# Performance work log

Measured on AMD Instinct MI355X. Metric: run time of the kernel, lower is better.

Reference implementation:

```python
import jax, jax.numpy as jnp
import numpy as np
import math

B, S, D, H = 2, 2048, 1024, 16
DK = D // H

def setup_inputs() -> dict:
    key = jax.random.key(0)
    ks = jax.random.split(key, 12)
    sc = 1.0 / math.sqrt(D)
    q = jax.random.normal(ks[0], (B, S, D), jnp.float32)
    k = jax.random.normal(ks[1], (B, S, D), jnp.float32)
    v = jax.random.normal(ks[2], (B, S, D), jnp.float32)
    # causal mask, broadcast over batch and heads; 0 -> masked (filled with -100)
    mask = jnp.tril(jnp.ones((S, S), jnp.int32))[None, None, :, :]
    w_q = jax.random.normal(ks[3], (D, D), jnp.float32) * sc
    b_q = jnp.zeros((D,), jnp.float32)
    w_k = jax.random.normal(ks[4], (D, D), jnp.float32) * sc
    b_k = jnp.zeros((D,), jnp.float32)
    w_v = jax.random.normal(ks[5], (D, D), jnp.float32) * sc
    b_v = jnp.zeros((D,), jnp.float32)
    w_0 = jax.random.normal(ks[6], (D, D), jnp.float32) * sc
    b_0 = jnp.zeros((D,), jnp.float32)
    return {"q": q, "k": k, "v": v, "mask": mask,
            "w_q": w_q, "b_q": b_q, "w_k": w_k, "b_k": b_k,
            "w_v": w_v, "b_v": b_v, "w_0": w_0, "b_0": b_0}

def reference(q, k, v, mask, w_q, b_q, w_k, b_k, w_v, b_v, w_0, b_0):
    # projections (nn.Linear: x @ W^T + b)
    query = q @ w_q.T + b_q              # [B,S,D]
    key_ = k @ w_k.T + b_k
    value = v @ w_v.T + b_v
    # split heads -> [B,H,S,DK]
    def split(x):
        return x.reshape(B, S, H, DK).transpose(0, 2, 1, 3)
    Q, K, V = split(query), split(key_), split(value)
    scores = jnp.einsum('bhqd,bhkd->bhqk', Q, K) / math.sqrt(DK)
    scores = jnp.where(mask == 0, jnp.float32(-100.0), scores)
    attn = jax.nn.softmax(scores, axis=-1)   # dropout p=0.0 -> identity
    out = jnp.einsum('bhqk,bhkd->bhqd', attn, V)  # [B,H,S,DK]
    out = out.transpose(0, 2, 1, 3).reshape(B, S, D)
    return out @ w_0.T + b_0
```

## Files before the change

### kernel.cpp

```cpp
#include <hip/hip_runtime.h>


namespace {

typedef unsigned short u16;
typedef short bf16x8 __attribute__((ext_vector_type(8)));
typedef float f32x4 __attribute__((ext_vector_type(4)));

constexpr int Bz = 2, Sq = 2048, Dm = 1024, Hh = 16, Dk = 64;
constexpr int Mr = Bz * Sq;

__device__ __forceinline__ u16 bf_rne(float f, float* hif) {
  unsigned u = __float_as_uint(f);
  unsigned r = (u + 0x7fffu + ((u >> 16) & 1u)) >> 16;
  if (hif) *hif = __uint_as_float(r << 16);
  return (u16)r;
}

__device__ __forceinline__ void global_load_lds16(const u16* g, u16* lds) {
  __builtin_amdgcn_global_load_lds(
      (const __attribute__((address_space(1))) void*)g,
      (__attribute__((address_space(3))) void*)lds, 16, 0, 0);
}

struct ConvArgs {
  const float* s[7]; u16* hi[7]; u16* lo[7]; int n[7];
};

__global__ __launch_bounds__(256)
void convert_hilo(ConvArgs a) {
  const int z = blockIdx.y;
  const int n = a.n[z];
  const int i = (blockIdx.x * 256 + threadIdx.x) * 4;
  if (i >= n) return;
  const float4 v = *(const float4*)(a.s[z] + i);
  float hf;
  ushort4 h, l;
  h.x = bf_rne(v.x, &hf); l.x = bf_rne(v.x - hf, nullptr);
  h.y = bf_rne(v.y, &hf); l.y = bf_rne(v.y - hf, nullptr);
  h.z = bf_rne(v.z, &hf); l.z = bf_rne(v.z - hf, nullptr);
  h.w = bf_rne(v.w, &hf); l.w = bf_rne(v.w - hf, nullptr);
  *(ushort4*)(a.hi[z] + i) = h;
  *(ushort4*)(a.lo[z] + i) = l;
}

template<int OUT>
__device__ __forceinline__ void gemm_split_body(
    const u16* __restrict__ Ahi, const u16* __restrict__ Alo,
    const u16* __restrict__ Bhi, const u16* __restrict__ Blo,
    const float* __restrict__ bias, float scale,
    u16* __restrict__ Yh, u16* __restrict__ Yl, float* __restrict__ Yf)
{
  constexpr int K = 1024;
  __shared__ u16 lAh[4096], lAl[4096], lBh[4096], lBl[4096];

  const int t = threadIdx.x;
  const int w = t >> 6, l = t & 63;
  const int m0 = blockIdx.x * 128, n0 = blockIdx.y * 128;
  const int wm = (w >> 1) * 64, wn = (w & 1) * 64;
  const int kg = l >> 4, lr = l & 15;

  f32x4 acc[4][4] = {};

  for (int k0 = 0; k0 < K; k0 += 32) {
#pragma unroll
    for (int is = 0; is < 2; ++is) {
      const int s = is * 256 + w * 64 + l;
      const int row = s & 127, g = s >> 7;
      const size_t aoff = (size_t)(m0 + row) * K + k0 + g * 8;
      const size_t boff = (size_t)(n0 + row) * K + k0 + g * 8;
      const int ldso = (is * 256 + w * 64) * 8;
      global_load_lds16(Ahi + aoff, &lAh[ldso]);
      global_load_lds16(Alo + aoff, &lAl[ldso]);
      global_load_lds16(Bhi + boff, &lBh[ldso]);
      global_load_lds16(Blo + boff, &lBl[ldso]);
    }
    __syncthreads();

    bf16x8 ah[4], al[4], bh[4], bl[4];
#pragma unroll
    for (int f = 0; f < 4; ++f) {
      const int ai = kg * 1024 + (wm + f * 16 + lr) * 8;
      const int bi = kg * 1024 + (wn + f * 16 + lr) * 8;
      ah[f] = *(const bf16x8*)&lAh[ai];
      al[f] = *(const bf16x8*)&lAl[ai];
      bh[f] = *(const bf16x8*)&lBh[bi];
      bl[f] = *(const bf16x8*)&lBl[bi];
    }
#pragma unroll
    for (int mf = 0; mf < 4; ++mf)
#pragma unroll
      for (int nf = 0; nf < 4; ++nf) {
        acc[mf][nf] = __builtin_amdgcn_mfma_f32_16x16x32_bf16(ah[mf], bh[nf], acc[mf][nf], 0, 0, 0);
        acc[mf][nf] = __builtin_amdgcn_mfma_f32_16x16x32_bf16(ah[mf], bl[nf], acc[mf][nf], 0, 0, 0);
        acc[mf][nf] = __builtin_amdgcn_mfma_f32_16x16x32_bf16(al[mf], bh[nf], acc[mf][nf], 0, 0, 0);
      }
    __syncthreads();
  }

#pragma unroll
  for (int mf = 0; mf < 4; ++mf)
#pragma unroll
    for (int nf = 0; nf < 4; ++nf) {
      const int n = n0 + wn + nf * 16 + lr;
      const float bv = bias[n];
#pragma unroll
      for (int r = 0; r < 4; ++r) {
        const int mm = m0 + wm + mf * 16 + kg * 4 + r;
        const float val = (acc[mf][nf][r] + bv) * scale;
        if (OUT == 2) {
          Yf[(size_t)mm * Dm + n] = val;
        } else {
          float hf;
          const u16 hi = bf_rne(val, &hf);
          const u16 lo = bf_rne(val - hf, nullptr);
          const int bb = mm >> 11, ss = mm & (Sq - 1);
          const int hh = n >> 6, dkk = n & (Dk - 1);
          size_t idx;
          if (OUT == 0) idx = ((size_t)(bb * Hh + hh) * Sq + ss) * Dk + dkk;
          else          idx = ((size_t)(bb * Hh + hh) * Dk + dkk) * Sq + ss;
          Yh[idx] = hi; Yl[idx] = lo;
        }
      }
    }
}

__global__ __launch_bounds__(256, 2)
void gemm_qkv_split(const u16* xqh, const u16* xql, const u16* xkh, const u16* xkl,
                    const u16* xvh, const u16* xvl,
                    const u16* wqh, const u16* wql, const u16* wkh, const u16* wkl,
                    const u16* wvh, const u16* wvl,
                    const float* bq, const float* bk, const float* bv,
                    u16* Qhi, u16* Qlo, u16* Khi, u16* Klo, u16* Vthi, u16* Vtlo)
{
  const int z = blockIdx.z;
  if (z == 0)
    gemm_split_body<0>(xqh, xql, wqh, wql, bq, 0.125f, Qhi, Qlo, nullptr);
  else if (z == 1)
    gemm_split_body<0>(xkh, xkl, wkh, wkl, bk, 1.0f, Khi, Klo, nullptr);
  else
    gemm_split_body<1>(xvh, xvl, wvh, wvl, bv, 1.0f, Vthi, Vtlo, nullptr);
}

__global__ __launch_bounds__(256, 2)
void gemm_out_split(const u16* Ah, const u16* Al, const u16* Bh, const u16* Bl,
                    const float* bias, float* Y)
{
  gemm_split_body<2>(Ah, Al, Bh, Bl, bias, 1.0f, nullptr, nullptr, Y);
}

__global__ __launch_bounds__(256, 2)
void attn_mfma(const u16* __restrict__ Qhi, const u16* __restrict__ Qlo,
               const u16* __restrict__ Khi, const u16* __restrict__ Klo,
               const u16* __restrict__ Vthi, const u16* __restrict__ Vtlo,
               u16* __restrict__ ctxh, u16* __restrict__ ctxl)
{
  __shared__ u16 stg[2 * 8192];
  __shared__ float Pld[4][16][36];

  const int qt = blockIdx.x, h = blockIdx.y, b = blockIdx.z;
  const int w = threadIdx.x >> 6, l = threadIdx.x & 63;
  const int lr = l & 15, g = l >> 4;
  const int q0 = qt * 64;
  const size_t hoff  = (size_t)(b * Hh + h) * Sq * Dk;
  const size_t hofft = (size_t)(b * Hh + h) * Dk * Sq;

  bf16x8 qh[2], ql[2];
  {
    const size_t qrow = hoff + (size_t)(q0 + 4 * lr + w) * Dk;
    qh[0] = *(const bf16x8*)(Qhi + qrow + 8 * g);
    qh[1] = *(const bf16x8*)(Qhi + qrow + 32 + 8 * g);
    ql[0] = *(const bf16x8*)(Qlo + qrow + 8 * g);
    ql[1] = *(const bf16x8*)(Qlo + qrow + 32 + 8 * g);
  }

  const int NT = 2 * (qt + 1);

  auto stage = [&](int t, int bb) {
    const int k0 = t * 32;
    u16* dst = stg + bb * 8192 + (w * 256) * 8;
#pragma unroll
    for (int jj = 0; jj < 4; ++jj) {
      const int s = jj * 64 + l;
      const u16* gp;
      if (w == 0)      gp = Khi  + hoff  + (size_t)(k0 + (s & 31)) * Dk + (s >> 5) * 8;
      else if (w == 1) gp = Klo  + hoff  + (size_t)(k0 + (s & 31)) * Dk + (s >> 5) * 8;
      else if (w == 2) gp = Vthi + hofft + (size_t)(s & 63) * Sq + k0 + (s >> 6) * 8;
      else             gp = Vtlo + hofft + (size_t)(s & 63) * Sq + k0 + (s >> 6) * 8;
      global_load_lds16(gp, dst + jj * 64 * 8);
    }
  };

  f32x4 O[4] = {};
  float m[4]    = {-1e30f, -1e30f, -1e30f, -1e30f};
  float lsum[4] = {0.f, 0.f, 0.f, 0.f};

  stage(0, 0);
  __syncthreads();

  for (int t = 0; t < NT; ++t) {
    const int bb = t & 1;
    const int k0 = t * 32;
    if (t + 1 < NT) stage(t + 1, bb ^ 1);

    const u16* sb = stg + bb * 8192;

    bf16x8 kh[2][2], kl[2][2];
#pragma unroll
    for (int c = 0; c < 2; ++c)
#pragma unroll
      for (int h16 = 0; h16 < 2; ++h16) {
        const int slot = (c * 4 + g) * 32 + h16 * 16 + lr;
        kh[h16][c] = *(const bf16x8*)(sb + slot * 8);
        kl[h16][c] = *(const bf16x8*)(sb + (256 + slot) * 8);
      }

    f32x4 Sv[2] = {};
#pragma unroll
    for (int c = 0; c < 2; ++c) {
      Sv[0] = __builtin_amdgcn_mfma_f32_16x16x32_bf16(qh[c], kh[0][c], Sv[0], 0, 0, 0);
      Sv[0] = __builtin_amdgcn_mfma_f32_16x16x32_bf16(qh[c], kl[0][c], Sv[0], 0, 0, 0);
      Sv[0] = __builtin_amdgcn_mfma_f32_16x16x32_bf16(ql[c], kh[0][c], Sv[0], 0, 0, 0);
      Sv[1] = __builtin_amdgcn_mfma_f32_16x16x32_bf16(qh[c], kh[1][c], Sv[1], 0, 0, 0);
      Sv[1] = __builtin_amdgcn_mfma_f32_16x16x32_bf16(qh[c], kl[1][c], Sv[1], 0, 0, 0);
      Sv[1] = __builtin_amdgcn_mfma_f32_16x16x32_bf16(ql[c], kh[1][c], Sv[1], 0, 0, 0);
    }

    if (k0 + 31 >= q0) {
#pragma unroll
      for (int h16 = 0; h16 < 2; ++h16) {
        const int kv = k0 + h16 * 16 + lr;
#pragma unroll
        for (int reg = 0; reg < 4; ++reg) {
          const int qq = q0 + 4 * (4 * g + reg) + w;
          if (kv > qq) Sv[h16][reg] = -3.0e38f;
        }
      }
    }

    float tmax[4], corr[4];
#pragma unroll
    for (int reg = 0; reg < 4; ++reg) tmax[reg] = fmaxf(Sv[0][reg], Sv[1][reg]);
#pragma unroll
    for (int d = 1; d < 16; d <<= 1)
#pragma unroll
      for (int reg = 0; reg < 4; ++reg)
        tmax[reg] = fmaxf(tmax[reg], __shfl_xor(tmax[reg], d));
#pragma unroll
    for (int reg = 0; reg < 4; ++reg) {
      const float mn = fmaxf(m[reg], tmax[reg]);
      corr[reg] = __expf(m[reg] - mn);
      m[reg] = mn;
    }
    f32x4 P0, P1;
    float psum[4];
#pragma unroll
    for (int reg = 0; reg < 4; ++reg) {
      P0[reg] = __expf(Sv[0][reg] - m[reg]);
      P1[reg] = __expf(Sv[1][reg] - m[reg]);
      psum[reg] = P0[reg] + P1[reg];
    }
#pragma unroll
    for (int d = 1; d < 16; d <<= 1)
#pragma unroll
      for (int reg = 0; reg < 4; ++reg)
        psum[reg] += __shfl_xor(psum[reg], d);
#pragma unroll
    for (int reg = 0; reg < 4; ++reg)
      lsum[reg] = lsum[reg] * corr[reg] + psum[reg];
#pragma unroll
    for (int dt = 0; dt < 4; ++dt)
#pragma unroll
      for (int reg = 0; reg < 4; ++reg)
        O[dt][reg] *= corr[reg];

#pragma unroll
    for (int reg = 0; reg < 4; ++reg) {
      Pld[w][4 * g + reg][lr]      = P0[reg];
      Pld[w][4 * g + reg][16 + lr] = P1[reg];
    }
    asm volatile("s_waitcnt lgkmcnt(0)" ::: "memory");
    float pa[8];
    *(float4*)&pa[0] = *(const float4*)&Pld[w][lr][8 * g];
    *(float4*)&pa[4] = *(const float4*)&Pld[w][lr][8 * g + 4];

    bf16x8 pah, pal;
#pragma unroll
    for (int j = 0; j < 8; ++j) {
      float hf;
      pah[j] = (short)bf_rne(pa[j], &hf);
      pal[j] = (short)bf_rne(pa[j] - hf, nullptr);
    }

#pragma unroll
    for (int dt = 0; dt < 4; ++dt) {
      const int vslot = 512 + g * 64 + dt * 16 + lr;
      const bf16x8 vh = *(const bf16x8*)(sb + vslot * 8);
      const bf16x8 vl = *(const bf16x8*)(sb + (vslot + 256) * 8);
      O[dt] = __builtin_amdgcn_mfma_f32_16x16x32_bf16(pah, vh, O[dt], 0, 0, 0);
      O[dt] = __builtin_amdgcn_mfma_f32_16x16x32_bf16(pah, vl, O[dt], 0, 0, 0);
      O[dt] = __builtin_amdgcn_mfma_f32_16x16x32_bf16(pal, vh, O[dt], 0, 0, 0);
    }

    __syncthreads();
  }

  float inv[4];
#pragma unroll
  for (int reg = 0; reg < 4; ++reg) inv[reg] = 1.0f / lsum[reg];
#pragma unroll
  for (int dt = 0; dt < 4; ++dt)
#pragma unroll
    for (int reg = 0; reg < 4; ++reg) {
      const int qq = q0 + 4 * (4 * g + reg) + w;
      const float o = O[dt][reg] * inv[reg];
      float hf;
      const u16 hi = bf_rne(o, &hf);
      const u16 lo = bf_rne(o - hf, nullptr);
      const size_t idx = ((size_t)(b * Sq + qq) << 10) + h * Dk + dt * 16 + lr;
      ctxh[idx] = hi;
      ctxl[idx] = lo;
    }
}

}

extern "C" void kernel_launch(void* const* d_in, const int* in_sizes, int n_in,
                              void* d_out, int out_size, void* d_ws, size_t ws_size,
                              hipStream_t stream)
{
  (void)in_sizes; (void)n_in; (void)out_size;

  const float* q   = (const float*)d_in[0];
  const float* k   = (const float*)d_in[1];
  const float* v   = (const float*)d_in[2];
  const float* w_q = (const float*)d_in[4];
  const float* b_q = (const float*)d_in[5];
  const float* w_k = (const float*)d_in[6];
  const float* b_k = (const float*)d_in[7];
  const float* w_v = (const float*)d_in[8];
  const float* b_v = (const float*)d_in[9];
  const float* w_0 = (const float*)d_in[10];
  const float* b_0 = (const float*)d_in[11];
  float* out = (float*)d_out;

  const size_t MB = 1024 * 1024;
  const size_t NACT = (size_t)Mr * Dm;
  const size_t NW   = (size_t)Dm * Dm;
  if (ws_size < 112 * MB) return;

  char* ws = (char*)d_ws;
  u16* xqh = (u16*)(ws + 0*MB);  u16* xql = (u16*)(ws + 8*MB);
  u16* xkh = (u16*)(ws + 16*MB); u16* xkl = (u16*)(ws + 24*MB);
  u16* xvh = (u16*)(ws + 32*MB); u16* xvl = (u16*)(ws + 40*MB);
  u16* ctxh = (u16*)(ws + 0*MB); u16* ctxl = (u16*)(ws + 8*MB);
  u16* wqh = (u16*)(ws + 48*MB); u16* wql = (u16*)(ws + 50*MB);
  u16* wkh = (u16*)(ws + 52*MB); u16* wkl = (u16*)(ws + 54*MB);
  u16* wvh = (u16*)(ws + 56*MB); u16* wvl = (u16*)(ws + 58*MB);
  u16* w0h = (u16*)(ws + 60*MB); u16* w0l = (u16*)(ws + 62*MB);
  u16* Qhi  = (u16*)(ws + 64*MB); u16* Qlo  = (u16*)(ws + 72*MB);
  u16* Khi  = (u16*)(ws + 80*MB); u16* Klo  = (u16*)(ws + 88*MB);
  u16* Vthi = (u16*)(ws + 96*MB); u16* Vtlo = (u16*)(ws + 104*MB);

  ConvArgs ca;
  ca.s[0] = q;   ca.hi[0] = xqh; ca.lo[0] = xql; ca.n[0] = (int)NACT;
  ca.s[1] = k;   ca.hi[1] = xkh; ca.lo[1] = xkl; ca.n[1] = (int)NACT;
  ca.s[2] = v;   ca.hi[2] = xvh; ca.lo[2] = xvl; ca.n[2] = (int)NACT;
  ca.s[3] = w_q; ca.hi[3] = wqh; ca.lo[3] = wql; ca.n[3] = (int)NW;
  ca.s[4] = w_k; ca.hi[4] = wkh; ca.lo[4] = wkl; ca.n[4] = (int)NW;
  ca.s[5] = w_v; ca.hi[5] = wvh; ca.lo[5] = wvl; ca.n[5] = (int)NW;
  ca.s[6] = w_0; ca.hi[6] = w0h; ca.lo[6] = w0l; ca.n[6] = (int)NW;

  convert_hilo<<<dim3(NACT / 1024, 7), 256, 0, stream>>>(ca);

  gemm_qkv_split<<<dim3(Mr / 128, Dm / 128, 3), 256, 0, stream>>>(
      xqh, xql, xkh, xkl, xvh, xvl,
      wqh, wql, wkh, wkl, wvh, wvl,
      b_q, b_k, b_v, Qhi, Qlo, Khi, Klo, Vthi, Vtlo);

  attn_mfma<<<dim3(Sq / 64, Hh, Bz), 256, 0, stream>>>(
      Qhi, Qlo, Khi, Klo, Vthi, Vtlo, ctxh, ctxl);

  gemm_out_split<<<dim3(Mr / 128, Dm / 128), 256, 0, stream>>>(
      ctxh, ctxl, w0h, w0l, b_0, out);
}
```

Before: 570.5 us.

## Transpose attention MFMA orientation to keep P in registers via lane shuffles

The attention kernel swaps MFMA operand order so each lane owns one query row. This turns row max/sum reductions into two cross-group shuffles, and P is rearranged for the PV MFMA with register shuffles instead of an LDS round-trip. Score accumulation is split into two independent chains to expose MFMA parallelism. Output stores become vectorised ushort4, V-transpose GEMM stores are vectorised, bf16 conversion uses the library intrinsic, and attention occupancy is raised to 3 blocks per SIMD, which risks register pressure or spilling.

Measured after the change: 486.0 us. 14.8% less time.

```diff
diff --git a/kernel.cpp b/kernel.cpp
--- a/kernel.cpp
+++ b/kernel.cpp
@@ -1,20 +1,23 @@
 #include <hip/hip_runtime.h>
+#include <hip/hip_bf16.h>
 
 
 namespace {
 
 typedef unsigned short u16;
+typedef unsigned int u32;
 typedef short bf16x8 __attribute__((ext_vector_type(8)));
 typedef float f32x4 __attribute__((ext_vector_type(4)));
+typedef int i32x4 __attribute__((ext_vector_type(4)));
 
 constexpr int Bz = 2, Sq = 2048, Dm = 1024, Hh = 16, Dk = 64;
 constexpr int Mr = Bz * Sq;
 
-__device__ __forceinline__ u16 bf_rne(float f, float* hif) {
-  unsigned u = __float_as_uint(f);
-  unsigned r = (u + 0x7fffu + ((u >> 16) & 1u)) >> 16;
-  if (hif) *hif = __uint_as_float(r << 16);
-  return (u16)r;
+__device__ __forceinline__ u16 bfh(float f) {
+  return __bfloat16_as_ushort(__float2bfloat16(f));
+}
+__device__ __forceinline__ float bfup(u16 u) {
+  return __uint_as_float((u32)u << 16);
 }
 
 __device__ __forceinline__ void global_load_lds16(const u16* g, u16* lds) {
@@ -34,12 +37,11 @@
   const int i = (blockIdx.x * 256 + threadIdx.x) * 4;
   if (i >= n) return;
   const float4 v = *(const float4*)(a.s[z] + i);
-  float hf;
   ushort4 h, l;
-  h.x = bf_rne(v.x, &hf); l.x = bf_rne(v.x - hf, nullptr);
-  h.y = bf_rne(v.y, &hf); l.y = bf_rne(v.y - hf, nullptr);
-  h.z = bf_rne(v.z, &hf); l.z = bf_rne(v.z - hf, nullptr);
-  h.w = bf_rne(v.w, &hf); l.w = bf_rne(v.w - hf, nullptr);
+  h.x = bfh(v.x); l.x = bfh(v.x - bfup(h.x));
+  h.y = bfh(v.y); l.y = bfh(v.y - bfup(h.y));
+  h.z = bfh(v.z); l.z = bfh(v.z - bfup(h.z));
+  h.w = bfh(v.w); l.w = bfh(v.w - bfup(h.w));
   *(ushort4*)(a.hi[z] + i) = h;
   *(ushort4*)(a.lo[z] + i) = l;
 }
@@ -104,22 +106,35 @@
     for (int nf = 0; nf < 4; ++nf) {
       const int n = n0 + wn + nf * 16 + lr;
       const float bv = bias[n];
-#pragma unroll
-      for (int r = 0; r < 4; ++r) {
-        const int mm = m0 + wm + mf * 16 + kg * 4 + r;
-        const float val = (acc[mf][nf][r] + bv) * scale;
-        if (OUT == 2) {
-          Yf[(size_t)mm * Dm + n] = val;
+      const int mbase = m0 + wm + mf * 16 + kg * 4;
+      if (OUT == 2) {
+#pragma unroll
+        for (int r = 0; r < 4; ++r)
+          Yf[(size_t)(mbase + r) * Dm + n] = (acc[mf][nf][r] + bv) * scale;
+      } else {
+        u16 hi[4], lo[4];
+#pragma unroll
+        for (int r = 0; r < 4; ++r) {
+          const float val = (acc[mf][nf][r] + bv) * scale;
+          hi[r] = bfh(val);
+          lo[r] = bfh(val - bfup(hi[r]));
+        }
+        const int bb = mbase >> 11;
+        const int hh = n >> 6, dkk = n & (Dk - 1);
+        if (OUT == 0) {
+          const size_t base = ((size_t)(bb * Hh + hh) * Sq + (mbase & (Sq - 1))) * Dk + dkk;
+#pragma unroll
+          for (int r = 0; r < 4; ++r) {
+            Yh[base + (size_t)r * Dk] = hi[r];
+            Yl[base + (size_t)r * Dk] = lo[r];
+          }
         } else {
-          float hf;
-          const u16 hi = bf_rne(val, &hf);
-          const u16 lo = bf_rne(val - hf, nullptr);
-          const int bb = mm >> 11, ss = mm & (Sq - 1);
-          const int hh = n >> 6, dkk = n & (Dk - 1);
-          size_t idx;
-          if (OUT == 0) idx = ((size_t)(bb * Hh + hh) * Sq + ss) * Dk + dkk;
-          else          idx = ((size_t)(bb * Hh + hh) * Dk + dkk) * Sq + ss;
-          Yh[idx] = hi; Yl[idx] = lo;
+          const size_t base = ((size_t)(bb * Hh + hh) * Dk + dkk) * Sq + (mbase & (Sq - 1));
+          ushort4 H, L;
+          H.x = hi[0]; H.y = hi[1]; H.z = hi[2]; H.w = hi[3];
+          L.x = lo[0]; L.y = lo[1]; L.z = lo[2]; L.w = lo[3];
+          *(ushort4*)(Yh + base) = H;
+          *(ushort4*)(Yl + base) = L;
         }
       }
     }
@@ -149,25 +164,25 @@
   gemm_split_body<2>(Ah, Al, Bh, Bl, bias, 1.0f, nullptr, nullptr, Y);
 }
 
-__global__ __launch_bounds__(256, 2)
+__global__ __launch_bounds__(256, 3)
 void attn_mfma(const u16* __restrict__ Qhi, const u16* __restrict__ Qlo,
                const u16* __restrict__ Khi, const u16* __restrict__ Klo,
                const u16* __restrict__ Vthi, const u16* __restrict__ Vtlo,
                u16* __restrict__ ctxh, u16* __restrict__ ctxl)
 {
   __shared__ u16 stg[2 * 8192];
-  __shared__ float Pld[4][16][36];
 
   const int qt = blockIdx.x, h = blockIdx.y, b = blockIdx.z;
   const int w = threadIdx.x >> 6, l = threadIdx.x & 63;
   const int lr = l & 15, g = l >> 4;
   const int q0 = qt * 64;
+  const int myq = q0 + w + 4 * lr;
   const size_t hoff  = (size_t)(b * Hh + h) * Sq * Dk;
   const size_t hofft = (size_t)(b * Hh + h) * Dk * Sq;
 
   bf16x8 qh[2], ql[2];
   {
-    const size_t qrow = hoff + (size_t)(q0 + 4 * lr + w) * Dk;
+    const size_t qrow = hoff + (size_t)myq * Dk;
     qh[0] = *(const bf16x8*)(Qhi + qrow + 8 * g);
     qh[1] = *(const bf16x8*)(Qhi + qrow + 32 + 8 * g);
     ql[0] = *(const bf16x8*)(Qlo + qrow + 8 * g);
@@ -192,8 +207,11 @@
   };
 
   f32x4 O[4] = {};
-  float m[4]    = {-1e30f, -1e30f, -1e30f, -1e30f};
-  float lsum[4] = {0.f, 0.f, 0.f, 0.f};
+  float m = -1e30f, lsum = 0.f;
+
+  const int hsel = g >> 1;
+  const int src0 = lr + ((g & 1) << 5);
+  const int src1 = src0 + 16;
 
   stage(0, 0);
   __syncthreads();
@@ -215,112 +233,115 @@
         kl[h16][c] = *(const bf16x8*)(sb + (256 + slot) * 8);
       }
 
-    f32x4 Sv[2] = {};
-#pragma unroll
-    for (int c = 0; c < 2; ++c) {
-      Sv[0] = __builtin_amdgcn_mfma_f32_16x16x32_bf16(qh[c], kh[0][c], Sv[0], 0, 0, 0);
-      Sv[0] = __builtin_amdgcn_mfma_f32_16x16x32_bf16(qh[c], kl[0][c], Sv[0], 0, 0, 0);
-      Sv[0] = __builtin_amdgcn_mfma_f32_16x16x32_bf16(ql[c], kh[0][c], Sv[0], 0, 0, 0);
-      Sv[1] = __builtin_amdgcn_mfma_f32_16x16x32_bf16(qh[c], kh[1][c], Sv[1], 0, 0, 0);
-      Sv[1] = __builtin_amdgcn_mfma_f32_16x16x32_bf16(qh[c], kl[1][c], Sv[1], 0, 0, 0);
-      Sv[1] = __builtin_amdgcn_mfma_f32_16x16x32_bf16(ql[c], kh[1][c], Sv[1], 0, 0, 0);
+    f32x4 Sv[2];
+#pragma unroll
+    for (int h16 = 0; h16 < 2; ++h16) {
+      f32x4 sa = {}, sb2 = {};
+      sa  = __builtin_amdgcn_mfma_f32_16x16x32_bf16(kh[h16][0], qh[0], sa, 0, 0, 0);
+      sa  = __builtin_amdgcn_mfma_f32_16x16x32_bf16(kh[h16][0], ql[0], sa, 0, 0, 0);
+      sa  = __builtin_amdgcn_mfma_f32_16x16x32_bf16(kl[h16][0], qh[0], sa, 0, 0, 0);
+      sb2 = __builtin_amdgcn_mfma_f32_16x16x32_bf16(kh[h16][1], qh[1], sb2, 0, 0, 0);
+      sb2 = __builtin_amdgcn_mfma_f32_16x16x32_bf16(kh[h16][1], ql[1], sb2, 0, 0, 0);
+      sb2 = __builtin_amdgcn_mfma_f32_16x16x32_bf16(kl[h16][1], qh[1], sb2, 0, 0, 0);
+      Sv[h16] = sa + sb2;
     }
 
     if (k0 + 31 >= q0) {
 #pragma unroll
-      for (int h16 = 0; h16 < 2; ++h16) {
-        const int kv = k0 + h16 * 16 + lr;
+      for (int h16 = 0; h16 < 2; ++h16)
 #pragma unroll
         for (int reg = 0; reg < 4; ++reg) {
-          const int qq = q0 + 4 * (4 * g + reg) + w;
-          if (kv > qq) Sv[h16][reg] = -3.0e38f;
+          const int kv = k0 + h16 * 16 + 4 * g + reg;
+          if (kv > myq) Sv[h16][reg] = -3.0e38f;
         }
+    }
+
+    float tmax = Sv[0][0];
+#pragma unroll
+    for (int r = 1; r < 4; ++r) tmax = fmaxf(tmax, Sv[0][r]);
+#pragma unroll
+    for (int r = 0; r < 4; ++r) tmax = fmaxf(tmax, Sv[1][r]);
+    tmax = fmaxf(tmax, __shfl_xor(tmax, 16));
+    tmax = fmaxf(tmax, __shfl_xor(tmax, 32));
+    const float mnew = fmaxf(m, tmax);
+    const float corr = __expf(m - mnew);
+    m = mnew;
+
+    float pp[2][4];
+    float psum = 0.f;
+#pragma unroll
+    for (int h16 = 0; h16 < 2; ++h16)
+#pragma unroll
+      for (int r = 0; r < 4; ++r) {
+        pp[h16][r] = __expf(Sv[h16][r] - m);
+        psum += pp[h16][r];
       }
-    }
-
-    float tmax[4], corr[4];
-#pragma unroll
-    for (int reg = 0; reg < 4; ++reg) tmax[reg] = fmaxf(Sv[0][reg], Sv[1][reg]);
-#pragma unroll
-    for (int d = 1; d < 16; d <<= 1)
-#pragma unroll
-      for (int reg = 0; reg < 4; ++reg)
-        tmax[reg] = fmaxf(tmax[reg], __shfl_xor(tmax[reg], d));
-#pragma unroll
-    for (int reg = 0; reg < 4; ++reg) {
-      const float mn = fmaxf(m[reg], tmax[reg]);
-      corr[reg] = __expf(m[reg] - mn);
-      m[reg] = mn;
-    }
-    f32x4 P0, P1;
-    float psum[4];
-#pragma unroll
-    for (int reg = 0; reg < 4; ++reg) {
-      P0[reg] = __expf(Sv[0][reg] - m[reg]);
-      P1[reg] = __expf(Sv[1][reg] - m[reg]);
-      psum[reg] = P0[reg] + P1[reg];
-    }
-#pragma unroll
-    for (int d = 1; d < 16; d <<= 1)
-#pragma unroll
-      for (int reg = 0; reg < 4; ++reg)
-        psum[reg] += __shfl_xor(psum[reg], d);
-#pragma unroll
-    for (int reg = 0; reg < 4; ++reg)
-      lsum[reg] = lsum[reg] * corr[reg] + psum[reg];
-#pragma unroll
-    for (int dt = 0; dt < 4; ++dt)
-#pragma unroll
-      for (int reg = 0; reg < 4; ++reg)
-        O[dt][reg] *= corr[reg];
-
-#pragma unroll
-    for (int reg = 0; reg < 4; ++reg) {
-      Pld[w][4 * g + reg][lr]      = P0[reg];
-      Pld[w][4 * g + reg][16 + lr] = P1[reg];
-    }
-    asm volatile("s_waitcnt lgkmcnt(0)" ::: "memory");
-    float pa[8];
-    *(float4*)&pa[0] = *(const float4*)&Pld[w][lr][8 * g];
-    *(float4*)&pa[4] = *(const float4*)&Pld[w][lr][8 * g + 4];
-
-    bf16x8 pah, pal;
-#pragma unroll
-    for (int j = 0; j < 8; ++j) {
-      float hf;
-      pah[j] = (short)bf_rne(pa[j], &hf);
-      pal[j] = (short)bf_rne(pa[j] - hf, nullptr);
-    }
+    psum += __shfl_xor(psum, 16);
+    psum += __shfl_xor(psum, 32);
+    lsum = lsum * corr + psum;
+#pragma unroll
+    for (int dt = 0; dt < 4; ++dt) O[dt] *= corr;
+
+    u32 Wh[4], Wl[4];
+#pragma unroll
+    for (int h16 = 0; h16 < 2; ++h16)
+#pragma unroll
+      for (int tp = 0; tp < 2; ++tp) {
+        const float p0 = pp[h16][2 * tp], p1 = pp[h16][2 * tp + 1];
+        const u16 h0 = bfh(p0), h1 = bfh(p1);
+        Wh[2 * h16 + tp] = (u32)h0 | ((u32)h1 << 16);
+        const u16 e0 = bfh(p0 - bfup(h0)), e1 = bfh(p1 - bfup(h1));
+        Wl[2 * h16 + tp] = (u32)e0 | ((u32)e1 << 16);
+      }
+
+    u32 a0 = (u32)__shfl((int)Wh[0], src0), a1 = (u32)__shfl((int)Wh[1], src0);
+    u32 a2 = (u32)__shfl((int)Wh[2], src0), a3 = (u32)__shfl((int)Wh[3], src0);
+    u32 b0 = (u32)__shfl((int)Wh[0], src1), b1 = (u32)__shfl((int)Wh[1], src1);
+    u32 b2 = (u32)__shfl((int)Wh[2], src1), b3 = (u32)__shfl((int)Wh[3], src1);
+    i32x4 th;
+    th.x = (int)(hsel ? a2 : a0); th.y = (int)(hsel ? a3 : a1);
+    th.z = (int)(hsel ? b2 : b0); th.w = (int)(hsel ? b3 : b1);
+    const bf16x8 pbh = __builtin_bit_cast(bf16x8, th);
+
+    a0 = (u32)__shfl((int)Wl[0], src0); a1 = (u32)__shfl((int)Wl[1], src0);
+    a2 = (u32)__shfl((int)Wl[2], src0); a3 = (u32)__shfl((int)Wl[3], src0);
+    b0 = (u32)__shfl((int)Wl[0], src1); b1 = (u32)__shfl((int)Wl[1], src1);
+    b2 = (u32)__shfl((int)Wl[2], src1); b3 = (u32)__shfl((int)Wl[3], src1);
+    i32x4 tl;
+    tl.x = (int)(hsel ? a2 : a0); tl.y = (int)(hsel ? a3 : a1);
+    tl.z = (int)(hsel ? b2 : b0); tl.w = (int)(hsel ? b3 : b1);
+    const bf16x8 pbl = __builtin_bit_cast(bf16x8, tl);
 
 #pragma unroll
     for (int dt = 0; dt < 4; ++dt) {
       const int vslot = 512 + g * 64 + dt * 16 + lr;
       const bf16x8 vh = *(const bf16x8*)(sb + vslot * 8);
       const bf16x8 vl = *(const bf16x8*)(sb + (vslot + 256) * 8);
-      O[dt] = __builtin_amdgcn_mfma_f32_16x16x32_bf16(pah, vh, O[dt], 0, 0, 0);
-      O[dt] = __builtin_amdgcn_mfma_f32_16x16x32_bf16(pah, vl, O[dt], 0, 0, 0);
-      O[dt] = __builtin_amdgcn_mfma_f32_16x16x32_bf16(pal, vh, O[dt], 0, 0, 0);
+      O[dt] = __builtin_amdgcn_mfma_f32_16x16x32_bf16(vh, pbh, O[dt], 0, 0, 0);
+      O[dt] = __builtin_amdgcn_mfma_f32_16x16x32_bf16(vh, pbl, O[dt], 0, 0, 0);
+      O[dt] = __builtin_amdgcn_mfma_f32_16x16x32_bf16(vl, pbh, O[dt], 0, 0, 0);
     }
 
     __syncthreads();
   }
 
-  float inv[4];
-#pragma unroll
-  for (int reg = 0; reg < 4; ++reg) inv[reg] = 1.0f / lsum[reg];
-#pragma unroll
-  for (int dt = 0; dt < 4; ++dt)
+  const float inv = 1.0f / lsum;
+  const size_t base = ((size_t)(b * Sq + myq) << 10) + h * Dk + 4 * g;
+#pragma unroll
+  for (int dt = 0; dt < 4; ++dt) {
+    u16 hi[4], lo[4];
 #pragma unroll
     for (int reg = 0; reg < 4; ++reg) {
-      const int qq = q0 + 4 * (4 * g + reg) + w;
-      const float o = O[dt][reg] * inv[reg];
-      float hf;
-      const u16 hi = bf_rne(o, &hf);
-      const u16 lo = bf_rne(o - hf, nullptr);
-      const size_t idx = ((size_t)(b * Sq + qq) << 10) + h * Dk + dt * 16 + lr;
-      ctxh[idx] = hi;
-      ctxl[idx] = lo;
-    }
+      const float o = O[dt][reg] * inv;
+      hi[reg] = bfh(o);
+      lo[reg] = bfh(o - bfup(hi[reg]));
+    }
+    ushort4 H, L;
+    H.x = hi[0]; H.y = hi[1]; H.z = hi[2]; H.w = hi[3];
+    L.x = lo[0]; L.y = lo[1]; L.z = lo[2]; L.w = lo[3];
+    *(ushort4*)(ctxh + base + dt * 16) = H;
+    *(ushort4*)(ctxl + base + dt * 16) = L;
+  }
 }
 
 }
```
